# Kernel optimization log

Measured on AMD Instinct MI355X. Metric: run time of the kernel, lower is better.

## Reference

```python
import jax, jax.numpy as jnp
import numpy as np

B, S, DM = 4, 2048, 1024
H, D = 16, 64  # nb_head, size_per_head
NEG = 1e12


def setup_inputs() -> dict:
    key = jax.random.key(0)
    ks = jax.random.split(key, 8)
    return {
        "Q_seq": jax.random.normal(ks[0], (B, S, DM), dtype=jnp.float32),
        "K_seq": jax.random.normal(ks[1], (B, S, DM), dtype=jnp.float32),
        "V_seq": jax.random.normal(ks[2], (B, S, DM), dtype=jnp.float32),
        "Q_len": jax.random.randint(ks[3], (B, 1), 0, S, dtype=jnp.int32),
        "V_len": jax.random.randint(ks[4], (B, 1), 0, S, dtype=jnp.int32),
        "WQ": jax.random.normal(ks[5], (DM, H * D), dtype=jnp.float32) * 0.02,
        "WK": jax.random.normal(ks[6], (DM, H * D), dtype=jnp.float32) * 0.02,
        "WV": jax.random.normal(ks[7], (DM, H * D), dtype=jnp.float32) * 0.02,
    }


def reference(Q_seq, K_seq, V_seq, Q_len, V_len, WQ, WK, WV):
    b, sq, _ = Q_seq.shape
    sk = K_seq.shape[1]
    # project and split heads -> [B, H, S, D]
    q = (Q_seq @ WQ).reshape(b, sq, H, D).transpose(0, 2, 1, 3)
    k = (K_seq @ WK).reshape(b, sk, H, D).transpose(0, 2, 1, 3)
    v = (V_seq @ WV).reshape(b, sk, H, D).transpose(0, 2, 1, 3)
    # scores [B, H, Sq, Sk]
    A = jnp.einsum("bhqd,bhkd->bhqk", q, k) / jnp.sqrt(jnp.float32(D))
    # key-length mask: positions t < V_len are valid (1 - cumsum(one_hot))
    kmask = (jnp.arange(sk)[None, :] < V_len[:, 0:1]).astype(A.dtype)  # [B, Sk]
    A = A - (1.0 - kmask)[:, None, None, :] * NEG
    A = jax.nn.softmax(A, axis=-1)
    O = jnp.einsum("bhqk,bhkd->bhqd", A, v)
    O = O.transpose(0, 2, 1, 3).reshape(b, sq, H * D)
    # query-length mask (multiplicative)
    qmask = (jnp.arange(sq)[None, :] < Q_len[:, 0:1]).astype(O.dtype)  # [B, Sq]
    return O * qmask[:, :, None]
```

## Files before the change

kernel.cpp:

```cpp
#include <hip/hip_runtime.h>
#include <hip/hip_bf16.h>
#include <math.h>

#define BATCH 4
#define SEQ   2048
#define DM    1024
#define NHEAD 16
#define HDIM  64
#define MROWS (BATCH*SEQ)

typedef float f32x4 __attribute__((ext_vector_type(4)));
typedef float f32x16 __attribute__((ext_vector_type(16)));
typedef short bf16x8 __attribute__((ext_vector_type(8)));
typedef unsigned int u32x4 __attribute__((ext_vector_type(4)));

typedef __attribute__((address_space(1))) unsigned int as1_u32;
typedef __attribute__((address_space(3))) unsigned int as3_u32;

__device__ __forceinline__ void gld16(const void* g, void* l) {
    __builtin_amdgcn_global_load_lds((const as1_u32*)g, (as3_u32*)l, 16, 0, 0);
}

__device__ __forceinline__ unsigned short f2bf(float f) {
    unsigned int u = __float_as_uint(f);
    u += 0x7FFFu + ((u >> 16) & 1u);
    return (unsigned short)(u >> 16);
}

__device__ __forceinline__ unsigned int pack2bf(float a, float b) {
    return (unsigned int)f2bf(a) | ((unsigned int)f2bf(b) << 16);
}

__device__ __forceinline__ float fexp2(float x) {
    float r;
    asm("v_exp_f32 %0, %1" : "=v"(r) : "v"(x));
    return r;
}

__device__ __forceinline__ unsigned int cvtpk2(float lo, float hi) {
    unsigned int r;
    asm("v_cvt_pk_bf16_f32 %0, %1, %2" : "=v"(r) : "v"(lo), "v"(hi));
    return r;
}

__device__ __forceinline__ int row_limit(int len, int lmode) {
    if (lmode == 0) return (len + 31) & ~31;
    if (lmode == 1) return (len <= 0) ? 0 : ((len + 63) & ~63);
    return (len <= 0) ? SEQ : ((len + 63) & ~63);
}

__global__ __launch_bounds__(256) void convx3_kernel(const float* __restrict__ Q,
                                                     const float* __restrict__ K,
                                                     const float* __restrict__ V,
                                                     unsigned short* __restrict__ Xq,
                                                     unsigned short* __restrict__ Xk,
                                                     unsigned short* __restrict__ Xv,
                                                     const int* __restrict__ Qlen,
                                                     const int* __restrict__ Vlen,
                                                     int zoff) {
    const int z = blockIdx.y + zoff;
    const float* in = (z == 0) ? Q : (z == 1) ? K : V;
    unsigned short* out = (z == 0) ? Xq : (z == 1) ? Xk : Xv;
    int i = blockIdx.x * 256 + threadIdx.x;
    int row = i >> 7;
    int b = row >> 11, s = row & 2047;
    int lim = (z == 0) ? row_limit(Qlen[b], 0) : row_limit(Vlen[b], z);
    if (s >= lim) return;
    const float4* p = reinterpret_cast<const float4*>(in) + (size_t)i * 2;
    float4 a = p[0], v = p[1];
    uint4 r;
    r.x = pack2bf(a.x, a.y);
    r.y = pack2bf(a.z, a.w);
    r.z = pack2bf(v.x, v.y);
    r.w = pack2bf(v.z, v.w);
    reinterpret_cast<uint4*>(out)[i] = r;
}

__global__ __launch_bounds__(256) void convw3_kernel(const float* __restrict__ WQ,
                                                     const float* __restrict__ WK,
                                                     const float* __restrict__ WV,
                                                     unsigned short* __restrict__ Oq,
                                                     unsigned short* __restrict__ Ok,
                                                     unsigned short* __restrict__ Ov,
                                                     int zoff) {
    const int z = blockIdx.z + zoff;
    const float* in = (z == 0) ? WQ : (z == 1) ? WK : WV;
    unsigned short* out = (z == 0) ? Oq : (z == 1) ? Ok : Ov;
    const float scale = (z == 0) ? 0.125f * 1.44269504088896340736f : 1.0f;
    __shared__ float tile[64][65];
    int n0 = blockIdx.x * 64, k0 = blockIdx.y * 64;
    int tx = threadIdx.x, ty = threadIdx.y;
#pragma unroll
    for (int i = 0; i < 64; i += 4)
        tile[ty + i][tx] = in[(size_t)(k0 + ty + i) * DM + n0 + tx];
    __syncthreads();
#pragma unroll
    for (int i = 0; i < 64; i += 4)
        out[(size_t)(n0 + ty + i) * DM + k0 + tx] = f2bf(tile[tx][ty + i] * scale);
}

__global__ __launch_bounds__(256) void gemm3_kernel(const unsigned short* __restrict__ Xq,
                                                    const unsigned short* __restrict__ Xk,
                                                    const unsigned short* __restrict__ Xv,
                                                    const unsigned short* __restrict__ Wq,
                                                    const unsigned short* __restrict__ Wk,
                                                    const unsigned short* __restrict__ Wv,
                                                    unsigned short* __restrict__ qo,
                                                    unsigned short* __restrict__ ko,
                                                    unsigned short* __restrict__ vo,
                                                    const int* __restrict__ Qlen,
                                                    const int* __restrict__ Vlen,
                                                    int zoff) {
    const int z = blockIdx.z + zoff;
    const unsigned short* A = (z == 0) ? Xq : (z == 1) ? Xk : Xv;
    const unsigned short* Bt = (z == 0) ? Wq : (z == 1) ? Wk : Wv;
    unsigned short* out = (z == 0) ? qo : (z == 1) ? ko : vo;
    const int vmode = (z == 2);
    const int mt_ = (blockIdx.y >> 3) * 8 + blockIdx.x;
    const int nt_ = blockIdx.y & 7;
    const int m0 = mt_ << 7, n0 = nt_ << 7;
    {
        int b = m0 >> 11, s0 = m0 & 2047;
        int len = (z == 0) ? Qlen[b] : Vlen[b];
        if (s0 >= row_limit(len, z)) return;
    }
    __shared__ unsigned short lA[2][128 * 32];
    __shared__ unsigned short lB[2][128 * 32];
    const int tid = threadIdx.x, lane = tid & 63, wave = tid >> 6;
    const int wr = wave >> 1, wc = wave & 1;
    const int col = lane & 15, grp = lane >> 4;

    f32x4 acc[4][4] = {};

    const int srow = tid >> 2;
    const int sx = (tid & 3) ^ (srow & 3);
    const unsigned short* srcA0 = A + (size_t)(m0 + srow) * DM + sx * 8;
    const unsigned short* srcA1 = srcA0 + (size_t)64 * DM;
    const unsigned short* srcB0 = Bt + (size_t)(n0 + srow) * DM + sx * 8;
    const unsigned short* srcB1 = srcB0 + (size_t)64 * DM;

#define STAGEG(BF, K0) do {                                   \
        gld16(srcA0 + (K0), &lA[BF][wave * 512]);             \
        gld16(srcA1 + (K0), &lA[BF][2048 + wave * 512]);      \
        gld16(srcB0 + (K0), &lB[BF][wave * 512]);             \
        gld16(srcB1 + (K0), &lB[BF][2048 + wave * 512]);      \
    } while (0)

    STAGEG(0, 0);

    const int xs = (grp ^ (col & 3)) * 8;
    int bf = 0;
    for (int k0 = 0; k0 < DM; k0 += 32) {
        if (k0 + 32 < DM) {
            STAGEG(bf ^ 1, k0 + 32);
            asm volatile("s_waitcnt vmcnt(4)" ::: "memory");
        } else {
            asm volatile("s_waitcnt vmcnt(0)" ::: "memory");
        }
        __builtin_amdgcn_sched_barrier(0);
        __builtin_amdgcn_s_barrier();
        __builtin_amdgcn_sched_barrier(0);

        bf16x8 af[4], bfr[4];
#pragma unroll
        for (int mt = 0; mt < 4; mt++)
            af[mt] = *reinterpret_cast<const bf16x8*>(&lA[bf][(wr * 64 + mt * 16 + col) * 32 + xs]);
#pragma unroll
        for (int nt = 0; nt < 4; nt++)
            bfr[nt] = *reinterpret_cast<const bf16x8*>(&lB[bf][(wc * 64 + nt * 16 + col) * 32 + xs]);
#pragma unroll
        for (int mt = 0; mt < 4; mt++)
#pragma unroll
            for (int nt = 0; nt < 4; nt++)
                acc[mt][nt] = __builtin_amdgcn_mfma_f32_16x16x32_bf16(af[mt], bfr[nt], acc[mt][nt], 0, 0, 0);

        __builtin_amdgcn_sched_barrier(0);
        __builtin_amdgcn_s_barrier();
        __builtin_amdgcn_sched_barrier(0);
        bf ^= 1;
    }
#undef STAGEG

#pragma unroll
    for (int mt = 0; mt < 4; mt++) {
        int rowb = m0 + wr * 64 + mt * 16 + grp * 4;
#pragma unroll
        for (int nt = 0; nt < 4; nt++) {
            int c = n0 + wc * 64 + nt * 16 + col;
            int h = c >> 6, d = c & 63;
            if (vmode == 0) {
#pragma unroll
                for (int r = 0; r < 4; r++) {
                    int rr = rowb + r;
                    int b = rr >> 11, s = rr & 2047;
                    out[((((size_t)(b * NHEAD + h)) << 11) + s) * HDIM + d] = f2bf(acc[mt][nt][r]);
                }
            } else {
                int b = rowb >> 11, s = rowb & 2047;
                uint2 pk;
                pk.x = pack2bf(acc[mt][nt][0], acc[mt][nt][1]);
                pk.y = pack2bf(acc[mt][nt][2], acc[mt][nt][3]);
                *reinterpret_cast<uint2*>(
                    &out[(((size_t)(b * NHEAD + h)) * HDIM + d) * SEQ + s]) = pk;
            }
        }
    }
}

__global__ __launch_bounds__(512) void flash_kernel(const unsigned short* __restrict__ qm,
                                                    const unsigned short* __restrict__ km,
                                                    const unsigned short* __restrict__ vtm,
                                                    const int* __restrict__ Qlen,
                                                    const int* __restrict__ Vlen,
                                                    float* __restrict__ out) {
    const int raw = blockIdx.x;
    const int x = raw & 7, y = raw >> 3;
    const int qt = y & 15, z = y >> 4;
    const int h = x + ((z & 1) << 3);
    const int b = z >> 1;
    const int q0 = qt << 7;
    const int lane = threadIdx.x & 63, wv = threadIdx.x >> 6;
    const int qw = wv & 3, kw = wv >> 2;
    const int qI = lane & 31, hi = lane >> 5;
    const int ql = Qlen[b], vl = Vlen[b];
    const int qrow = q0 + qw * 32 + qI;

    if (q0 >= ql) {
        int r = threadIdx.x >> 2;
        int c0 = (threadIdx.x & 3) * 16;
        float* p = out + (size_t)(b * SEQ + q0 + r) * DM + h * HDIM + c0;
        float4 z4 = {0.f, 0.f, 0.f, 0.f};
        reinterpret_cast<float4*>(p)[0] = z4;
        reinterpret_cast<float4*>(p)[1] = z4;
        reinterpret_cast<float4*>(p)[2] = z4;
        reinterpret_cast<float4*>(p)[3] = z4;
        return;
    }

    const bool uniform = (vl <= 0);
    const int eff = uniform ? SEQ : vl;
    const int nkv = (eff + 63) >> 6;

    const size_t hb = ((size_t)(b * NHEAD + h)) << 11;
    const unsigned short* qbase = qm + hb * HDIM;
    const unsigned short* kbase = km + hb * HDIM;
    const unsigned short* vbase = vtm + hb * HDIM;

    __shared__ __align__(16) unsigned short lsK[2][2][64 * 64];
    __shared__ __align__(16) unsigned short lsV[2][2][64 * 64];

    const int r8 = lane >> 3, cs = lane & 7;
    const int sx = cs ^ r8;
    const size_t offK0 = (size_t)(qw * 16 + r8) * HDIM + sx * 8;
    const size_t offK1 = offK0 + (size_t)8 * HDIM;
    const size_t offV0 = (size_t)(qw * 16 + r8) * SEQ + sx * 8;
    const size_t offV1 = offV0 + (size_t)8 * SEQ;

#define STAGE(BF, T) do {                                                \
        const int kv0_ = (T) << 6;                                       \
        const unsigned short* gk_ = kbase + (size_t)kv0_ * HDIM;         \
        const unsigned short* gv_ = vbase + kv0_;                        \
        gld16(gk_ + offK0, &lsK[kw][BF][(qw * 16) * 64]);                \
        gld16(gk_ + offK1, &lsK[kw][BF][(qw * 16 + 8) * 64]);            \
        gld16(gv_ + offV0, &lsV[kw][BF][(qw * 16) * 64]);                \
        gld16(gv_ + offV1, &lsV[kw][BF][(qw * 16 + 8) * 64]);            \
    } while (0)

    bf16x8 qB[4];
#pragma unroll
    for (int sp = 0; sp < 4; sp++)
        qB[sp] = *reinterpret_cast<const bf16x8*>(&qbase[(size_t)qrow * HDIM + sp * 16 + hi * 8]);

    f32x16 o_acc2[2] = {};
    float m = -3.0e38f, l = 0.f;
    const int q7 = qI & 7;

    const int rounds = (nkv + 1) >> 1;
    if (kw < nkv) STAGE(0, kw);

    int bf = 0;
    for (int r = 0; r < rounds; r++) {
        const int tcur = 2 * r + kw;
        const int tnext = tcur + 2;
        if (tnext < nkv) {
            STAGE(bf ^ 1, tnext);
            asm volatile("s_waitcnt vmcnt(4)" ::: "memory");
        } else {
            asm volatile("s_waitcnt vmcnt(0)" ::: "memory");
        }
        __builtin_amdgcn_sched_barrier(0);
        __builtin_amdgcn_s_barrier();
        __builtin_amdgcn_sched_barrier(0);

        if (tcur < nkv) {
            const int kv0 = tcur << 6;

            f32x16 st2[2] = {};
            const unsigned short* Kb = &lsK[kw][bf][0];
#pragma unroll
            for (int kt = 0; kt < 2; kt++)
#pragma unroll
                for (int sp = 0; sp < 4; sp++) {
                    int xsk = (sp * 2 + hi) ^ q7;
                    bf16x8 ka = *reinterpret_cast<const bf16x8*>(&Kb[(kt * 32 + qI) * 64 + xsk * 8]);
                    st2[kt] = __builtin_amdgcn_mfma_f32_32x32x16_bf16(ka, qB[sp], st2[kt], 0, 0, 0);
                }

            if (uniform) {
#pragma unroll
                for (int t = 0; t < 2; t++)
#pragma unroll
                    for (int rr = 0; rr < 16; rr++) st2[t][rr] = 0.f;
            } else if (kv0 + 64 > eff) {
#pragma unroll
                for (int t = 0; t < 2; t++)
#pragma unroll
                    for (int rr = 0; rr < 16; rr++)
                        if (kv0 + t * 32 + (rr & 3) + 8 * (rr >> 2) + 4 * hi >= eff)
                            st2[t][rr] = -1e30f;
            }

            float tm8[8];
#pragma unroll
            for (int rr = 0; rr < 8; rr++)
                tm8[rr] = fmaxf(fmaxf(st2[0][rr], st2[0][rr + 8]), fmaxf(st2[1][rr], st2[1][rr + 8]));
            float tm4[4];
#pragma unroll
            for (int rr = 0; rr < 4; rr++) tm4[rr] = fmaxf(tm8[rr], tm8[rr + 4]);
            float mx = fmaxf(fmaxf(tm4[0], tm4[1]), fmaxf(tm4[2], tm4[3]));
            mx = fmaxf(mx, __shfl_xor(mx, 32));
            if (!__all(mx - m <= 8.0f)) {
                float mnew = fmaxf(m, mx);
                float sc = fexp2(m - mnew);
                l *= sc;
                o_acc2[0] *= sc;
                o_acc2[1] *= sc;
                m = mnew;
            }
#pragma unroll
            for (int t = 0; t < 2; t++)
#pragma unroll
                for (int rr = 0; rr < 16; rr++) st2[t][rr] = fexp2(st2[t][rr] - m);
            float ts8[8];
#pragma unroll
            for (int rr = 0; rr < 8; rr++)
                ts8[rr] = (st2[0][rr] + st2[0][rr + 8]) + (st2[1][rr] + st2[1][rr + 8]);
            float ts4[4];
#pragma unroll
            for (int rr = 0; rr < 4; rr++) ts4[rr] = ts8[rr] + ts8[rr + 4];
            float rs = (ts4[0] + ts4[1]) + (ts4[2] + ts4[3]);
            rs += __shfl_xor(rs, 32);
            l += rs;

            unsigned int pk[2][8];
#pragma unroll
            for (int t = 0; t < 2; t++)
#pragma unroll
                for (int p = 0; p < 8; p++)
                    pk[t][p] = cvtpk2(st2[t][2 * p], st2[t][2 * p + 1]);

            const unsigned short* Vb = &lsV[kw][bf][0];
#pragma unroll
            for (int ks = 0; ks < 4; ks++) {
                const int t = ks >> 1, c = (ks & 1) * 4;
                unsigned int sel0 = pk[t][c], sel1 = pk[t][c + 1];
                unsigned int sel2 = pk[t][c + 2], sel3 = pk[t][c + 3];
                unsigned int sendA = hi ? sel0 : sel2;
                unsigned int sendB = hi ? sel1 : sel3;
                unsigned int gotA = __shfl_xor(sendA, 32);
                unsigned int gotB = __shfl_xor(sendB, 32);
                u32x4 u;
                u[0] = hi ? gotA : sel0;
                u[1] = hi ? gotB : sel1;
                u[2] = hi ? sel2 : gotA;
                u[3] = hi ? sel3 : gotB;
                bf16x8 pB = __builtin_bit_cast(bf16x8, u);
                int xsv = (ks * 2 + hi) ^ q7;
#pragma unroll
                for (int dt = 0; dt < 2; dt++) {
                    bf16x8 va = *reinterpret_cast<const bf16x8*>(&Vb[(dt * 32 + qI) * 64 + xsv * 8]);
                    o_acc2[dt] = __builtin_amdgcn_mfma_f32_32x32x16_bf16(va, pB, o_acc2[dt], 0, 0, 0);
                }
            }
        }

        __builtin_amdgcn_sched_barrier(0);
        __builtin_amdgcn_s_barrier();
        __builtin_amdgcn_sched_barrier(0);
        bf ^= 1;
    }
#undef STAGE

    float* base = (float*)&lsK[0][0][0];
    float* osc = base;
    float* mls = base + 512 * 17;
    const int self = (wv << 6) + lane;
    const int peer = ((wv ^ 4) << 6) + lane;
    f32x16 o_keep = (kw == 0) ? o_acc2[0] : o_acc2[1];
    f32x16 o_give = (kw == 0) ? o_acc2[1] : o_acc2[0];
    mls[self * 2] = m;
    mls[self * 2 + 1] = l;
#pragma unroll
    for (int i = 0; i < 16; i++) osc[self * 17 + i] = o_give[i];
    __syncthreads();
    const float m2 = mls[peer * 2], l2 = mls[peer * 2 + 1];
    const float msh = fmaxf(m, m2);
    const float f1 = fexp2(m - msh), f2 = fexp2(m2 - msh);
    const float rl = 1.0f / (f1 * l + f2 * l2);
    const bool live = (qrow < ql);
    float* obase = out + (size_t)(b * SEQ + qrow) * DM + h * HDIM;
#pragma unroll
    for (int a = 0; a < 4; a++) {
        float4 val;
        float v0 = f1 * o_keep[4 * a + 0] + f2 * osc[peer * 17 + 4 * a + 0];
        float v1 = f1 * o_keep[4 * a + 1] + f2 * osc[peer * 17 + 4 * a + 1];
        float v2 = f1 * o_keep[4 * a + 2] + f2 * osc[peer * 17 + 4 * a + 2];
        float v3 = f1 * o_keep[4 * a + 3] + f2 * osc[peer * 17 + 4 * a + 3];
        val.x = live ? v0 * rl : 0.f;
        val.y = live ? v1 * rl : 0.f;
        val.z = live ? v2 * rl : 0.f;
        val.w = live ? v3 * rl : 0.f;
        *reinterpret_cast<float4*>(&obase[kw * 32 + a * 8 + hi * 4]) = val;
    }
}

extern "C" void kernel_launch(void* const* d_in, const int* in_sizes, int n_in,
                              void* d_out, int out_size, void* d_ws, size_t ws_size,
                              hipStream_t stream) {
    const float* Q_seq = (const float*)d_in[0];
    const float* K_seq = (const float*)d_in[1];
    const float* V_seq = (const float*)d_in[2];
    const int* Q_len = (const int*)d_in[3];
    const int* V_len = (const int*)d_in[4];
    const float* WQ = (const float*)d_in[5];
    const float* WK = (const float*)d_in[6];
    const float* WV = (const float*)d_in[7];
    float* out = (float*)d_out;

    const size_t XN = (size_t)MROWS * DM;
    const size_t WN = (size_t)DM * DM;
    const size_t need_fast = (6 * XN + 3 * WN) * sizeof(unsigned short);

    const int cx_grid = MROWS * DM / 8 / 256;
    dim3 cw_grid(DM / 64, DM / 64, 3), cw_blk(64, 4);
    dim3 g_grid(8, 64, 3), g_blk(256);

    if (ws_size >= need_fast) {
        unsigned short* Xq = (unsigned short*)d_ws;
        unsigned short* Xk = Xq + XN;
        unsigned short* Xv = Xk + XN;
        unsigned short* Wq = Xv + XN;
        unsigned short* Wk = Wq + WN;
        unsigned short* Wv = Wk + WN;
        unsigned short* qb = Wv + WN;
        unsigned short* kb = qb + XN;
        unsigned short* vtb = kb + XN;

        convx3_kernel<<<dim3(cx_grid, 3), 256, 0, stream>>>(Q_seq, K_seq, V_seq,
                                                            Xq, Xk, Xv, Q_len, V_len, 0);
        convw3_kernel<<<cw_grid, cw_blk, 0, stream>>>(WQ, WK, WV, Wq, Wk, Wv, 0);
        gemm3_kernel<<<g_grid, g_blk, 0, stream>>>(Xq, Xk, Xv, Wq, Wk, Wv,
                                                   qb, kb, vtb, Q_len, V_len, 0);
        flash_kernel<<<dim3(1024), 512, 0, stream>>>(qb, kb, vtb, Q_len, V_len, out);
    } else {
        unsigned short* Xbuf = (unsigned short*)d_ws;
        unsigned short* Wt = Xbuf + XN;
        unsigned short* qb = Wt + WN;
        unsigned short* kb = qb + XN;
        unsigned short* vtb = kb + XN;
        dim3 cw1(DM / 64, DM / 64, 1);
        dim3 g1(8, 64, 1);
        for (int z = 0; z < 3; z++) {
            convx3_kernel<<<dim3(cx_grid, 1), 256, 0, stream>>>(Q_seq, K_seq, V_seq,
                                                                Xbuf, Xbuf, Xbuf, Q_len, V_len, z);
            convw3_kernel<<<cw1, cw_blk, 0, stream>>>(WQ, WK, WV, Wt, Wt, Wt, z);
            gemm3_kernel<<<g1, g_blk, 0, stream>>>(Xbuf, Xbuf, Xbuf, Wt, Wt, Wt,
                                                   qb, kb, vtb, Q_len, V_len, z);
        }
        flash_kernel<<<dim3(1024), 512, 0, stream>>>(qb, kb, vtb, Q_len, V_len, out);
    }
}
```

Baseline: 128.4 us.

## Retile QKV projection GEMM to 128x64 tiles with two-wave blocks

The projection GEMM moves from 256-thread blocks computing 128x128 tiles to 128-thread blocks computing 128x64 tiles, doubling the grid along N. The LDS staging layout and the grouped block-to-tile mapping both change, and the XOR swizzle on LDS reads is dropped. The aim is more blocks and better occupancy and load balance, especially with early-exit masked rows. In exchange, operand reuse per block drops, global traffic for A rises, and the unswizzled LDS reads may cause bank conflicts.

```diff
diff --git a/kernel.cpp b/kernel.cpp
--- a/kernel.cpp
+++ b/kernel.cpp
@@ -99,7 +99,7 @@
         out[(size_t)(n0 + ty + i) * DM + k0 + tx] = f2bf(tile[tx][ty + i] * scale);
 }
 
-__global__ __launch_bounds__(256) void gemm3_kernel(const unsigned short* __restrict__ Xq,
+__global__ __launch_bounds__(128) void gemm3_kernel(const unsigned short* __restrict__ Xq,
                                                     const unsigned short* __restrict__ Xk,
                                                     const unsigned short* __restrict__ Xv,
                                                     const unsigned short* __restrict__ Wq,
@@ -116,44 +116,40 @@
     const unsigned short* Bt = (z == 0) ? Wq : (z == 1) ? Wk : Wv;
     unsigned short* out = (z == 0) ? qo : (z == 1) ? ko : vo;
     const int vmode = (z == 2);
-    const int mt_ = (blockIdx.y >> 3) * 8 + blockIdx.x;
-    const int nt_ = blockIdx.y & 7;
-    const int m0 = mt_ << 7, n0 = nt_ << 7;
+    const int m0 = blockIdx.y << 7;
+    const int n0 = blockIdx.x << 6;
     {
         int b = m0 >> 11, s0 = m0 & 2047;
         int len = (z == 0) ? Qlen[b] : Vlen[b];
         if (s0 >= row_limit(len, z)) return;
     }
     __shared__ unsigned short lA[2][128 * 32];
-    __shared__ unsigned short lB[2][128 * 32];
+    __shared__ unsigned short lB[2][64 * 32];
     const int tid = threadIdx.x, lane = tid & 63, wave = tid >> 6;
-    const int wr = wave >> 1, wc = wave & 1;
     const int col = lane & 15, grp = lane >> 4;
 
     f32x4 acc[4][4] = {};
 
-    const int srow = tid >> 2;
-    const int sx = (tid & 3) ^ (srow & 3);
-    const unsigned short* srcA0 = A + (size_t)(m0 + srow) * DM + sx * 8;
-    const unsigned short* srcA1 = srcA0 + (size_t)64 * DM;
-    const unsigned short* srcB0 = Bt + (size_t)(n0 + srow) * DM + sx * 8;
-    const unsigned short* srcB1 = srcB0 + (size_t)64 * DM;
-
-#define STAGEG(BF, K0) do {                                   \
-        gld16(srcA0 + (K0), &lA[BF][wave * 512]);             \
-        gld16(srcA1 + (K0), &lA[BF][2048 + wave * 512]);      \
-        gld16(srcB0 + (K0), &lB[BF][wave * 512]);             \
-        gld16(srcB1 + (K0), &lB[BF][2048 + wave * 512]);      \
+    const int r16 = lane >> 2, sg = (lane & 3) * 8;
+    const unsigned short* srcA = A + (size_t)(m0 + wave * 64 + r16) * DM + sg;
+    const unsigned short* srcB = Bt + (size_t)(n0 + wave * 32 + r16) * DM + sg;
+
+#define STAGEG(BF, K0) do {                                               \
+        gld16(srcA + (K0),           &lA[BF][(wave * 64) * 32]);          \
+        gld16(srcA + 16 * DM + (K0), &lA[BF][(wave * 64 + 16) * 32]);     \
+        gld16(srcA + 32 * DM + (K0), &lA[BF][(wave * 64 + 32) * 32]);     \
+        gld16(srcA + 48 * DM + (K0), &lA[BF][(wave * 64 + 48) * 32]);     \
+        gld16(srcB + (K0),           &lB[BF][(wave * 32) * 32]);          \
+        gld16(srcB + 16 * DM + (K0), &lB[BF][(wave * 32 + 16) * 32]);     \
     } while (0)
 
     STAGEG(0, 0);
 
-    const int xs = (grp ^ (col & 3)) * 8;
     int bf = 0;
     for (int k0 = 0; k0 < DM; k0 += 32) {
         if (k0 + 32 < DM) {
             STAGEG(bf ^ 1, k0 + 32);
-            asm volatile("s_waitcnt vmcnt(4)" ::: "memory");
+            asm volatile("s_waitcnt vmcnt(6)" ::: "memory");
         } else {
             asm volatile("s_waitcnt vmcnt(0)" ::: "memory");
         }
@@ -164,10 +160,10 @@
         bf16x8 af[4], bfr[4];
 #pragma unroll
         for (int mt = 0; mt < 4; mt++)
-            af[mt] = *reinterpret_cast<const bf16x8*>(&lA[bf][(wr * 64 + mt * 16 + col) * 32 + xs]);
+            af[mt] = *reinterpret_cast<const bf16x8*>(&lA[bf][(wave * 64 + mt * 16 + col) * 32 + grp * 8]);
 #pragma unroll
         for (int nt = 0; nt < 4; nt++)
-            bfr[nt] = *reinterpret_cast<const bf16x8*>(&lB[bf][(wc * 64 + nt * 16 + col) * 32 + xs]);
+            bfr[nt] = *reinterpret_cast<const bf16x8*>(&lB[bf][(nt * 16 + col) * 32 + grp * 8]);
 #pragma unroll
         for (int mt = 0; mt < 4; mt++)
 #pragma unroll
@@ -183,10 +179,10 @@
 
 #pragma unroll
     for (int mt = 0; mt < 4; mt++) {
-        int rowb = m0 + wr * 64 + mt * 16 + grp * 4;
+        int rowb = m0 + wave * 64 + mt * 16 + grp * 4;
 #pragma unroll
         for (int nt = 0; nt < 4; nt++) {
-            int c = n0 + wc * 64 + nt * 16 + col;
+            int c = n0 + nt * 16 + col;
             int h = c >> 6, d = c & 63;
             if (vmode == 0) {
 #pragma unroll
@@ -443,7 +439,7 @@
 
     const int cx_grid = MROWS * DM / 8 / 256;
     dim3 cw_grid(DM / 64, DM / 64, 3), cw_blk(64, 4);
-    dim3 g_grid(8, 64, 3), g_blk(256);
+    dim3 g_grid(16, 64, 3), g_blk(128);
 
     if (ws_size >= need_fast) {
         unsigned short* Xq = (unsigned short*)d_ws;
@@ -469,7 +465,7 @@
         unsigned short* kb = qb + XN;
         unsigned short* vtb = kb + XN;
         dim3 cw1(DM / 64, DM / 64, 1);
-        dim3 g1(8, 64, 1);
+        dim3 g1(16, 64, 1);
         for (int z = 0; z < 3; z++) {
             convx3_kernel<<<dim3(cx_grid, 1), 256, 0, stream>>>(Q_seq, K_seq, V_seq,
                                                                 Xbuf, Xbuf, Xbuf, Q_len, V_len, z);
```

Result: slower. 131.2 us (+2.2%).

## Split KV loop across four wave groups with two-stage merge in flash kernel

Applied to the files above, without the earlier changes.

Doubles the flash-attention block to 1024 threads so that four key/value wave groups, instead of two, each process an interleaved subset of KV tiles. LDS staging buffers double to hold four groups, and the final softmax merge becomes a two-stage pairwise reduction through shared memory. The aim is to shorten each block's serial KV loop and expose more parallelism per query tile. In exchange, LDS use doubles (128KB), which limits occupancy to one block per CU, and the epilogue needs extra barriers and exchange steps.

```diff
diff --git a/kernel.cpp b/kernel.cpp
--- a/kernel.cpp
+++ b/kernel.cpp
@@ -207,33 +207,32 @@
     }
 }
 
-__global__ __launch_bounds__(512) void flash_kernel(const unsigned short* __restrict__ qm,
-                                                    const unsigned short* __restrict__ km,
-                                                    const unsigned short* __restrict__ vtm,
-                                                    const int* __restrict__ Qlen,
-                                                    const int* __restrict__ Vlen,
-                                                    float* __restrict__ out) {
+__global__ __launch_bounds__(1024) void flash_kernel(const unsigned short* __restrict__ qm,
+                                                     const unsigned short* __restrict__ km,
+                                                     const unsigned short* __restrict__ vtm,
+                                                     const int* __restrict__ Qlen,
+                                                     const int* __restrict__ Vlen,
+                                                     float* __restrict__ out) {
     const int raw = blockIdx.x;
     const int x = raw & 7, y = raw >> 3;
     const int qt = y & 15, z = y >> 4;
     const int h = x + ((z & 1) << 3);
     const int b = z >> 1;
     const int q0 = qt << 7;
-    const int lane = threadIdx.x & 63, wv = threadIdx.x >> 6;
+    const int tid = threadIdx.x;
+    const int lane = tid & 63, wv = tid >> 6;
     const int qw = wv & 3, kw = wv >> 2;
     const int qI = lane & 31, hi = lane >> 5;
     const int ql = Qlen[b], vl = Vlen[b];
     const int qrow = q0 + qw * 32 + qI;
 
     if (q0 >= ql) {
-        int r = threadIdx.x >> 2;
-        int c0 = (threadIdx.x & 3) * 16;
+        int r = tid >> 3;
+        int c0 = (tid & 7) * 8;
         float* p = out + (size_t)(b * SEQ + q0 + r) * DM + h * HDIM + c0;
         float4 z4 = {0.f, 0.f, 0.f, 0.f};
         reinterpret_cast<float4*>(p)[0] = z4;
         reinterpret_cast<float4*>(p)[1] = z4;
-        reinterpret_cast<float4*>(p)[2] = z4;
-        reinterpret_cast<float4*>(p)[3] = z4;
         return;
     }
 
@@ -246,14 +245,14 @@
     const unsigned short* kbase = km + hb * HDIM;
     const unsigned short* vbase = vtm + hb * HDIM;
 
-    __shared__ __align__(16) unsigned short lsK[2][2][64 * 64];
-    __shared__ __align__(16) unsigned short lsV[2][2][64 * 64];
+    __shared__ __align__(16) unsigned short lsK[4][2][64 * 64];
+    __shared__ __align__(16) unsigned short lsV[4][2][64 * 64];
 
     const int r8 = lane >> 3, cs = lane & 7;
-    const int sx = cs ^ r8;
-    const size_t offK0 = (size_t)(qw * 16 + r8) * HDIM + sx * 8;
+    const int sxs = cs ^ r8;
+    const size_t offK0 = (size_t)(qw * 16 + r8) * HDIM + sxs * 8;
     const size_t offK1 = offK0 + (size_t)8 * HDIM;
-    const size_t offV0 = (size_t)(qw * 16 + r8) * SEQ + sx * 8;
+    const size_t offV0 = (size_t)(qw * 16 + r8) * SEQ + sxs * 8;
     const size_t offV1 = offV0 + (size_t)8 * SEQ;
 
 #define STAGE(BF, T) do {                                                \
@@ -275,13 +274,13 @@
     float m = -3.0e38f, l = 0.f;
     const int q7 = qI & 7;
 
-    const int rounds = (nkv + 1) >> 1;
+    const int rounds = (nkv + 3) >> 2;
     if (kw < nkv) STAGE(0, kw);
 
     int bf = 0;
     for (int r = 0; r < rounds; r++) {
-        const int tcur = 2 * r + kw;
-        const int tnext = tcur + 2;
+        const int tcur = 4 * r + kw;
+        const int tnext = tcur + 4;
         if (tnext < nkv) {
             STAGE(bf ^ 1, tnext);
             asm volatile("s_waitcnt vmcnt(4)" ::: "memory");
@@ -391,36 +390,58 @@
     }
 #undef STAGE
 
-    float* base = (float*)&lsK[0][0][0];
-    float* osc = base;
-    float* mls = base + 512 * 17;
+    float* scr = (float*)&lsK[0][0][0];
     const int self = (wv << 6) + lane;
-    const int peer = ((wv ^ 4) << 6) + lane;
-    f32x16 o_keep = (kw == 0) ? o_acc2[0] : o_acc2[1];
-    f32x16 o_give = (kw == 0) ? o_acc2[1] : o_acc2[0];
-    mls[self * 2] = m;
-    mls[self * 2 + 1] = l;
-#pragma unroll
-    for (int i = 0; i < 16; i++) osc[self * 17 + i] = o_give[i];
     __syncthreads();
-    const float m2 = mls[peer * 2], l2 = mls[peer * 2 + 1];
-    const float msh = fmaxf(m, m2);
-    const float f1 = fexp2(m - msh), f2 = fexp2(m2 - msh);
-    const float rl = 1.0f / (f1 * l + f2 * l2);
+
+    const int dtk = kw & 1;
+    f32x16 keepA = o_acc2[dtk];
+    f32x16 giveA = o_acc2[dtk ^ 1];
+    float* oscA = scr;
+    float* mlA = scr + 1024 * 17;
+    mlA[self * 2] = m;
+    mlA[self * 2 + 1] = l;
+#pragma unroll
+    for (int i = 0; i < 16; i++) oscA[self * 17 + i] = giveA[i];
+    __syncthreads();
+    const int peerA = ((wv ^ 4) << 6) + lane;
+    float m2 = mlA[peerA * 2], l2 = mlA[peerA * 2 + 1];
+    float msh = fmaxf(m, m2);
+    float f1 = fexp2(m - msh), f2 = fexp2(m2 - msh);
+    float o16[16];
+#pragma unroll
+    for (int i = 0; i < 16; i++) o16[i] = f1 * keepA[i] + f2 * oscA[peerA * 17 + i];
+    float lA_ = f1 * l + f2 * l2;
+    float mA_ = msh;
+    __syncthreads();
+
+    const int qs = kw >> 1;
+    float* oscB = scr;
+    float* mlB = scr + 1024 * 9;
+    mlB[self * 2] = mA_;
+    mlB[self * 2 + 1] = lA_;
+#pragma unroll
+    for (int i = 0; i < 8; i++) oscB[self * 9 + i] = o16[(qs ^ 1) * 8 + i];
+    __syncthreads();
+    const int peerB = ((wv ^ 8) << 6) + lane;
+    float mB2 = mlB[peerB * 2], lB2 = mlB[peerB * 2 + 1];
+    float msh2 = fmaxf(mA_, mB2);
+    float g1 = fexp2(mA_ - msh2), g2 = fexp2(mB2 - msh2);
+    const float rl = 1.0f / (g1 * lA_ + g2 * lB2);
     const bool live = (qrow < ql);
     float* obase = out + (size_t)(b * SEQ + qrow) * DM + h * HDIM;
 #pragma unroll
-    for (int a = 0; a < 4; a++) {
+    for (int a2 = 0; a2 < 2; a2++) {
         float4 val;
-        float v0 = f1 * o_keep[4 * a + 0] + f2 * osc[peer * 17 + 4 * a + 0];
-        float v1 = f1 * o_keep[4 * a + 1] + f2 * osc[peer * 17 + 4 * a + 1];
-        float v2 = f1 * o_keep[4 * a + 2] + f2 * osc[peer * 17 + 4 * a + 2];
-        float v3 = f1 * o_keep[4 * a + 3] + f2 * osc[peer * 17 + 4 * a + 3];
+        float v0 = g1 * o16[qs * 8 + a2 * 4 + 0] + g2 * oscB[peerB * 9 + a2 * 4 + 0];
+        float v1 = g1 * o16[qs * 8 + a2 * 4 + 1] + g2 * oscB[peerB * 9 + a2 * 4 + 1];
+        float v2 = g1 * o16[qs * 8 + a2 * 4 + 2] + g2 * oscB[peerB * 9 + a2 * 4 + 2];
+        float v3 = g1 * o16[qs * 8 + a2 * 4 + 3] + g2 * oscB[peerB * 9 + a2 * 4 + 3];
         val.x = live ? v0 * rl : 0.f;
         val.y = live ? v1 * rl : 0.f;
         val.z = live ? v2 * rl : 0.f;
         val.w = live ? v3 * rl : 0.f;
-        *reinterpret_cast<float4*>(&obase[kw * 32 + a * 8 + hi * 4]) = val;
+        *reinterpret_cast<float4*>(&obase[dtk * 32 + (2 * qs + a2) * 8 + hi * 4]) = val;
     }
 }
 
@@ -461,7 +482,7 @@
         convw3_kernel<<<cw_grid, cw_blk, 0, stream>>>(WQ, WK, WV, Wq, Wk, Wv, 0);
         gemm3_kernel<<<g_grid, g_blk, 0, stream>>>(Xq, Xk, Xv, Wq, Wk, Wv,
                                                    qb, kb, vtb, Q_len, V_len, 0);
-        flash_kernel<<<dim3(1024), 512, 0, stream>>>(qb, kb, vtb, Q_len, V_len, out);
+        flash_kernel<<<dim3(1024), 1024, 0, stream>>>(qb, kb, vtb, Q_len, V_len, out);
     } else {
         unsigned short* Xbuf = (unsigned short*)d_ws;
         unsigned short* Wt = Xbuf + XN;
@@ -477,6 +498,6 @@
             gemm3_kernel<<<g1, g_blk, 0, stream>>>(Xbuf, Xbuf, Xbuf, Wt, Wt, Wt,
                                                    qb, kb, vtb, Q_len, V_len, z);
         }
-        flash_kernel<<<dim3(1024), 512, 0, stream>>>(qb, kb, vtb, Q_len, V_len, out);
-    }
-}
+        flash_kernel<<<dim3(1024), 1024, 0, stream>>>(qb, kb, vtb, Q_len, V_len, out);
+    }
+}
```

After: 183.8 us. 1.43x slower.
